# Kernel tuning notes

Measured on AMD Instinct MI355X. Metric: run time of the kernel, lower is better.

## Reference

```python
import jax, jax.numpy as jnp
import numpy as np

GAMMA = 0.99
LAMBDA = 0.95
NU = 0.001
LOG_2PI = float(np.log(2.0 * np.pi))

B, T, H, R, C, A = 256, 64, 512, 32, 32, 64
H1, H2 = 1024, 1024
D = H + R * C  # critic input dim = hidden_state + flattened latent


def setup_inputs() -> dict:
    key = jax.random.key(0)
    ks = jax.random.split(key, 13)
    sc = lambda n: 1.0 / np.sqrt(n)
    return {
        "h": jax.random.normal(ks[0], (B, T, H), jnp.float32),
        "z": jax.random.normal(ks[1], (B, T, R, C), jnp.float32),
        "reward": jax.random.normal(ks[2], (B, T, 1), jnp.float32) * 0.1,
        "cont": jax.random.uniform(ks[3], (B, T, 1), jnp.float32),
        "action": jax.random.normal(ks[4], (B, T, A), jnp.float32),
        "a_mu": jax.random.normal(ks[5], (B, T, A), jnp.float32),
        "a_sigma": jax.random.uniform(ks[6], (B, T, A), jnp.float32) + 0.5,
        "W1": jax.random.normal(ks[7], (D, H1), jnp.float32) * sc(D),
        "b1": jnp.zeros((H1,), jnp.float32),
        "W2": jax.random.normal(ks[8], (H1, H2), jnp.float32) * sc(H1),
        "b2": jnp.zeros((H2,), jnp.float32),
        "W3": jax.random.normal(ks[9], (H2, 1), jnp.float32) * sc(H2),
        "b3": jnp.zeros((1,), jnp.float32),
    }


def _critic(h, z, W1, b1, W2, b2, W3, b3):
    # flatten latent [B,T,R,C] -> [B,T,R*C], concat with hidden state
    zf = z.reshape(z.shape[0], z.shape[1], -1)
    st = jnp.concatenate([h, zf], axis=-1)  # [B,T,D]
    x = jax.nn.silu(st @ W1 + b1)
    x = jax.nn.silu(x @ W2 + b2)
    return x @ W3 + b3  # [B,T,1]


def _r_lambda(value, reward, cont):
    # value/reward/cont: [B,T,1]; backward TD(lambda) recursion over time
    vt = value[..., 0].T   # [T,B] time-major
    rt = reward[..., 0].T
    ct = cont[..., 0].T

    def step(R_next, xs):
        r, c, v_next = xs
        R_cur = r + GAMMA * c * ((1.0 - LAMBDA) * v_next + LAMBDA * R_next)
        return R_cur, R_cur

    _, Rs = jax.lax.scan(step, vt[-1], (rt[:-1], ct[:-1], vt[1:]), reverse=True)
    R_lam = jnp.concatenate([Rs, vt[-1:]], axis=0)  # [T,B]
    return R_lam.T[..., None]  # [B,T,1]


def reference(h, z, reward, cont, action, a_mu, a_sigma, W1, b1, W2, b2, W3, b3):
    value = _critic(h, z, W1, b1, W2, b2, W3, b3)  # [B,T,1]
    # R_lambda uses detached value estimates
    R_lam = _r_lambda(jax.lax.stop_gradient(value), reward, cont)  # [B,T,1]
    advantage = R_lam - value  # [B,T,1]

    # Normal(mu, sigma) log_prob and entropy
    log_sig = jnp.log(a_sigma)
    log_prob = -0.5 * jnp.square((action - a_mu) / a_sigma) - log_sig - 0.5 * LOG_2PI  # [B,T,A]
    entropy = 0.5 + 0.5 * LOG_2PI + log_sig  # [B,T,A]

    loss_actor = -jnp.mean(
        log_prob * jax.lax.stop_gradient(advantage)
        + NU * jax.lax.stop_gradient(entropy)
    )
    loss_critic = jnp.mean(0.5 * jnp.square(value - jax.lax.stop_gradient(R_lam)))
    return jnp.stack([loss_actor, loss_critic])
```

## Files before the change

kernel.cpp:

```cpp
#include <hip/hip_runtime.h>
#include <hip/hip_bf16.h>
#include <stdint.h>

typedef short s8v  __attribute__((ext_vector_type(8)));
typedef float f4v  __attribute__((ext_vector_type(4)));

__device__ __forceinline__ unsigned short f2bf(float f) {
  unsigned int u = __float_as_uint(f);
  u += 0x7fffu + ((u >> 16) & 1u);
  return (unsigned short)(u >> 16);
}
__device__ __forceinline__ float bf2f(unsigned short u) {
  return __uint_as_float(((unsigned int)u) << 16);
}

#define GLOAD16(g, l)                                                          \
  __builtin_amdgcn_global_load_lds(                                            \
      (const __attribute__((address_space(1))) unsigned int*)(g),              \
      (__attribute__((address_space(3))) unsigned int*)(l), 16, 0, 0)

__global__ __launch_bounds__(256) void prep_x(const float* __restrict__ h,
                                              const float* __restrict__ z,
                                              unsigned short* __restrict__ X) {
  int idx = blockIdx.x * 256 + threadIdx.x;
  int m = idx / 192;
  int c = (idx - m * 192) * 8;
  const float* s = (c < 512) ? (h + (size_t)m * 512 + c)
                             : (z + (size_t)m * 1024 + (c - 512));
  f4v f0 = *(const f4v*)s;
  f4v f1 = *(const f4v*)(s + 4);
  s8v o;
  o[0] = (short)f2bf(f0[0]); o[1] = (short)f2bf(f0[1]);
  o[2] = (short)f2bf(f0[2]); o[3] = (short)f2bf(f0[3]);
  o[4] = (short)f2bf(f1[0]); o[5] = (short)f2bf(f1[1]);
  o[6] = (short)f2bf(f1[2]); o[7] = (short)f2bf(f1[3]);
  *(s8v*)(X + (size_t)m * 1536 + c) = o;
}

__global__ __launch_bounds__(256) void transpose_w(const float* __restrict__ W,
                                                   unsigned short* __restrict__ WT,
                                                   int K, int N) {
  __shared__ float tile[32][33];
  int tx = threadIdx.x & 31;
  int ty = threadIdx.x >> 5;
  int k0 = blockIdx.x * 32;
  int n0 = blockIdx.y * 32;
#pragma unroll
  for (int i = 0; i < 4; ++i)
    tile[ty + i * 8][tx] = W[(size_t)(k0 + ty + i * 8) * N + n0 + tx];
  __syncthreads();
#pragma unroll
  for (int i = 0; i < 4; ++i)
    WT[(size_t)(n0 + ty + i * 8) * K + k0 + tx] = f2bf(tile[tx][ty + i * 8]);
}

template<int K, bool FUSE>
__global__ __launch_bounds__(512) void gemm256(
    const unsigned short* __restrict__ A, const unsigned short* __restrict__ Bt,
    const float* __restrict__ bias, unsigned short* __restrict__ Cout,
    const float* __restrict__ W3, float* __restrict__ value) {
  constexpr int NOUT = 1024;
  constexpr int NT = K / 64;
  __shared__ char lds[131072];
  char* const A0 = lds;
  char* const B0 = lds + 32768;
  char* const A1 = lds + 65536;
  char* const B1 = lds + 98304;

  const int tid = threadIdx.x;
  const int w = tid >> 6, l = tid & 63;
  const int wr = w >> 2, wc = w & 3;
  const int tm = blockIdx.x * 256;
  const int tn = blockIdx.y * 256;
  const int l15 = l & 15, lh = l >> 4;

  const int sgrow = tid >> 3;
  const int sgk = ((tid & 7) ^ (sgrow & 7)) * 8;
  const unsigned short* Ag = A  + (size_t)(tm + sgrow) * K + sgk;
  const unsigned short* Bg = Bt + (size_t)(tn + sgrow) * K + sgk;
  const int wb = w * 1024;

  f4v acc[8][4];
#pragma unroll
  for (int i = 0; i < 8; ++i)
#pragma unroll
    for (int j = 0; j < 4; ++j) acc[i][j] = (f4v){0.f, 0.f, 0.f, 0.f};

#pragma unroll
  for (int i = 0; i < 4; ++i) {
    GLOAD16(Ag + (size_t)i * 64 * K, A0 + i * 8192 + wb);
    GLOAD16(Bg + (size_t)i * 64 * K, B0 + i * 8192 + wb);
  }
  asm volatile("s_waitcnt vmcnt(0)" ::: "memory");
  __builtin_amdgcn_s_barrier();

  auto iter = [&](int t, char* Ac, char* Bc, char* An, char* Bn) {
    if (t + 1 < NT) {
      const size_t ko = (size_t)(t + 1) * 64;
#pragma unroll
      for (int i = 0; i < 4; ++i) {
        GLOAD16(Ag + (size_t)i * 64 * K + ko, An + i * 8192 + wb);
        GLOAD16(Bg + (size_t)i * 64 * K + ko, Bn + i * 8192 + wb);
      }
    }
    s8v bf[4];
#pragma unroll
    for (int ph = 0; ph < 4; ++ph) {
      const int kk = ph >> 1, mh = ph & 1;
      const int k16 = kk * 4 + lh;
      if (mh == 0) {
#pragma unroll
        for (int ni = 0; ni < 4; ++ni) {
          const int row = wc * 64 + ni * 16 + l15;
          bf[ni] = *(const s8v*)(Bc + row * 128 + ((k16 ^ (row & 7)) << 4));
        }
      }
      s8v af[4];
#pragma unroll
      for (int mi = 0; mi < 4; ++mi) {
        const int row = wr * 128 + (mh * 4 + mi) * 16 + l15;
        af[mi] = *(const s8v*)(Ac + row * 128 + ((k16 ^ (row & 7)) << 4));
      }
      __builtin_amdgcn_s_setprio(1);
#pragma unroll
      for (int mi = 0; mi < 4; ++mi)
#pragma unroll
        for (int ni = 0; ni < 4; ++ni)
          acc[mh * 4 + mi][ni] = __builtin_amdgcn_mfma_f32_16x16x32_bf16(
              af[mi], bf[ni], acc[mh * 4 + mi][ni], 0, 0, 0);
      __builtin_amdgcn_s_setprio(0);
      __builtin_amdgcn_s_barrier();
    }
    asm volatile("s_waitcnt vmcnt(0)" ::: "memory");
    __builtin_amdgcn_s_barrier();
  };

  for (int t = 0; t < NT; t += 2) {
    iter(t,     A0, B0, A1, B1);
    iter(t + 1, A1, B1, A0, B0);
  }

  if constexpr (!FUSE) {
#pragma unroll
    for (int ni = 0; ni < 4; ++ni) {
      const int col = tn + wc * 64 + ni * 16 + l15;
      const float bb = bias[col];
#pragma unroll
      for (int mi = 0; mi < 8; ++mi) {
#pragma unroll
        for (int r = 0; r < 4; ++r) {
          const int row = tm + wr * 128 + mi * 16 + lh * 4 + r;
          float v = acc[mi][ni][r] + bb;
          v = v / (1.f + __expf(-v));
          Cout[(size_t)row * NOUT + col] = f2bf(v);
        }
      }
    }
  } else {
    float bb[4], w3[4];
#pragma unroll
    for (int ni = 0; ni < 4; ++ni) {
      const int col = tn + wc * 64 + ni * 16 + l15;
      bb[ni] = bias[col];
      w3[ni] = W3[col];
    }
#pragma unroll
    for (int mi = 0; mi < 8; ++mi) {
#pragma unroll
      for (int r = 0; r < 4; ++r) {
        float s = 0.f;
#pragma unroll
        for (int ni = 0; ni < 4; ++ni) {
          float v = acc[mi][ni][r] + bb[ni];
          v = v / (1.f + __expf(-v));
          s += v * w3[ni];
        }
        s += __shfl_xor(s, 1);
        s += __shfl_xor(s, 2);
        s += __shfl_xor(s, 4);
        s += __shfl_xor(s, 8);
        if (l15 == 0)
          atomicAdd(&value[tm + wr * 128 + mi * 16 + lh * 4 + r], s);
      }
    }
  }
}

__global__ void td_kernel(const float* __restrict__ value,
                          const float* __restrict__ reward,
                          const float* __restrict__ cont,
                          const float* __restrict__ b3,
                          float* __restrict__ adv, float* __restrict__ accs) {
  const int b = threadIdx.x;
  const float g = 0.99f, lam = 0.95f;
  const float vb = b3[0];
  float Rn = value[b * 64 + 63] + vb;
  adv[b * 64 + 63] = 0.f;
  float s = 0.f;
  for (int t = 62; t >= 0; --t) {
    const int i = b * 64 + t;
    float vn = value[i + 1] + vb;
    float R = reward[i] + g * cont[i] * ((1.f - lam) * vn + lam * Rn);
    float a = R - (value[i] + vb);
    adv[i] = a;
    s += a * a;
    Rn = R;
  }
#pragma unroll
  for (int off = 32; off; off >>= 1) s += __shfl_down(s, off);
  __shared__ float red[4];
  if ((threadIdx.x & 63) == 0) red[threadIdx.x >> 6] = s;
  __syncthreads();
  if (threadIdx.x == 0) accs[0] = red[0] + red[1] + red[2] + red[3];
}

__global__ __launch_bounds__(256) void actor_kernel(
    const float* __restrict__ action, const float* __restrict__ a_mu,
    const float* __restrict__ a_sigma, const float* __restrict__ adv,
    float* __restrict__ accs) {
  const float C1 = 0.91893853320467274f;
  const float NU = 0.001f;
  const size_t t = (size_t)blockIdx.x * 256 + threadIdx.x;
  const size_t base = t * 4;
  const int m = (int)(base >> 6);
  const float av = adv[m];
  f4v a = *(const f4v*)(action + base);
  f4v mu = *(const f4v*)(a_mu + base);
  f4v sg = *(const f4v*)(a_sigma + base);
  float s = 0.f;
#pragma unroll
  for (int j = 0; j < 4; ++j) {
    float d = (a[j] - mu[j]) / sg[j];
    float ls = __logf(sg[j]);
    float lp = -0.5f * d * d - ls - C1;
    s += lp * av + NU * (0.5f + C1 + ls);
  }
#pragma unroll
  for (int off = 32; off; off >>= 1) s += __shfl_down(s, off);
  __shared__ float red[4];
  if ((threadIdx.x & 63) == 0) red[threadIdx.x >> 6] = s;
  __syncthreads();
  if (threadIdx.x == 0) atomicAdd(&accs[1], red[0] + red[1] + red[2] + red[3]);
}

__global__ void fin_kernel(const float* __restrict__ accs, float* __restrict__ out) {
  out[0] = -accs[1] / 1048576.0f;
  out[1] = 0.5f * accs[0] / 16384.0f;
}

extern "C" void kernel_launch(void* const* d_in, const int* in_sizes, int n_in,
                              void* d_out, int out_size, void* d_ws, size_t ws_size,
                              hipStream_t stream) {
  const float* h       = (const float*)d_in[0];
  const float* z       = (const float*)d_in[1];
  const float* reward  = (const float*)d_in[2];
  const float* cont    = (const float*)d_in[3];
  const float* action  = (const float*)d_in[4];
  const float* a_mu    = (const float*)d_in[5];
  const float* a_sigma = (const float*)d_in[6];
  const float* W1      = (const float*)d_in[7];
  const float* b1      = (const float*)d_in[8];
  const float* W2      = (const float*)d_in[9];
  const float* b2      = (const float*)d_in[10];
  const float* W3      = (const float*)d_in[11];
  const float* b3      = (const float*)d_in[12];

  char* ws = (char*)d_ws;
  unsigned short* X   = (unsigned short*)(ws);
  unsigned short* W1T = (unsigned short*)(ws + 50331648);
  unsigned short* W2T = (unsigned short*)(ws + 53477376);
  unsigned short* X1  = (unsigned short*)(ws + 55574528);
  float* value = (float*)(ws + 89128960);
  float* adv   = (float*)(ws + 89194496);
  float* accs  = (float*)(ws + 89260032);

  hipMemsetAsync(value, 0, 131088, stream);
  prep_x<<<12288, 256, 0, stream>>>(h, z, X);
  transpose_w<<<dim3(48, 32), 256, 0, stream>>>(W1, W1T, 1536, 1024);
  transpose_w<<<dim3(32, 32), 256, 0, stream>>>(W2, W2T, 1024, 1024);
  gemm256<1536, false><<<dim3(64, 4), 512, 0, stream>>>(X, W1T, b1, X1, nullptr, nullptr);
  gemm256<1024, true><<<dim3(64, 4), 512, 0, stream>>>(X1, W2T, b2, nullptr, W3, value);
  td_kernel<<<1, 256, 0, stream>>>(value, reward, cont, b3, adv, accs);
  actor_kernel<<<1024, 256, 0, stream>>>(action, a_mu, a_sigma, adv, accs);
  fin_kernel<<<1, 1, 0, stream>>>(accs, (float*)d_out);
}
```

Measured before the change: 290.0 us.

## Interleave next-tile loads across MFMA phases and fuse TD with actor loss

The GEMM main loop no longer issues all prefetch loads for the next K-tile at the top of each iteration. It now spreads them across the four MFMA phases, one quarter-tile per phase, and waits only at the last phase, so global-to-LDS traffic overlaps more evenly with compute. Separately, the serial single-block TD(lambda) kernel and the actor reduction kernel are merged into one kernel with one block per batch row. Each block computes its row's advantages in shared memory and then reduces the actor loss for that row, which removes one launch and the global advantage buffer. The risks are extra barriers per phase in the GEMM and a single-thread serial recursion inside each block.

```diff
diff --git a/kernel.cpp b/kernel.cpp
--- a/kernel.cpp
+++ b/kernel.cpp
@@ -9,9 +9,6 @@
   unsigned int u = __float_as_uint(f);
   u += 0x7fffu + ((u >> 16) & 1u);
   return (unsigned short)(u >> 16);
-}
-__device__ __forceinline__ float bf2f(unsigned short u) {
-  return __uint_as_float(((unsigned int)u) << 16);
 }
 
 #define GLOAD16(g, l)                                                          \
@@ -62,10 +59,6 @@
   constexpr int NOUT = 1024;
   constexpr int NT = K / 64;
   __shared__ char lds[131072];
-  char* const A0 = lds;
-  char* const B0 = lds + 32768;
-  char* const A1 = lds + 65536;
-  char* const B1 = lds + 98304;
 
   const int tid = threadIdx.x;
   const int w = tid >> 6, l = tid & 63;
@@ -74,12 +67,20 @@
   const int tn = blockIdx.y * 256;
   const int l15 = l & 15, lh = l >> 4;
 
-  const int sgrow = tid >> 3;
-  const int sgk = ((tid & 7) ^ (sgrow & 7)) * 8;
-  const unsigned short* Ag = A  + (size_t)(tm + sgrow) * K + sgk;
-  const unsigned short* Bg = Bt + (size_t)(tn + sgrow) * K + sgk;
+  const int srow = tid >> 3;
+  const int sk = ((tid & 7) ^ (srow & 7)) * 8;
+  const unsigned short* Ag = A  + (size_t)(tm + srow) * K + sk;
+  const unsigned short* Bg = Bt + (size_t)(tn + srow) * K + sk;
   const int wb = w * 1024;
 
+  auto stage_ht = [&](int p, char* bufbase, int kt) {
+    const unsigned short* g =
+        (p < 2 ? Ag : Bg) + (size_t)(p & 1) * 128 * K + kt;
+    char* d = bufbase + p * 16384 + wb;
+    GLOAD16(g, d);
+    GLOAD16(g + (size_t)64 * K, d + 8192);
+  };
+
   f4v acc[8][4];
 #pragma unroll
   for (int i = 0; i < 8; ++i)
@@ -87,23 +88,18 @@
     for (int j = 0; j < 4; ++j) acc[i][j] = (f4v){0.f, 0.f, 0.f, 0.f};
 
 #pragma unroll
-  for (int i = 0; i < 4; ++i) {
-    GLOAD16(Ag + (size_t)i * 64 * K, A0 + i * 8192 + wb);
-    GLOAD16(Bg + (size_t)i * 64 * K, B0 + i * 8192 + wb);
-  }
+  for (int p = 0; p < 4; ++p) stage_ht(p, lds, 0);
   asm volatile("s_waitcnt vmcnt(0)" ::: "memory");
   __builtin_amdgcn_s_barrier();
 
-  auto iter = [&](int t, char* Ac, char* Bc, char* An, char* Bn) {
-    if (t + 1 < NT) {
-      const size_t ko = (size_t)(t + 1) * 64;
-#pragma unroll
-      for (int i = 0; i < 4; ++i) {
-        GLOAD16(Ag + (size_t)i * 64 * K + ko, An + i * 8192 + wb);
-        GLOAD16(Bg + (size_t)i * 64 * K + ko, Bn + i * 8192 + wb);
-      }
-    }
-    s8v bf[4];
+  s8v bf[4];
+  for (int t = 0; t < NT; ++t) {
+    char* const cb = lds + ((t & 1) ? 65536 : 0);
+    char* const nb = lds + ((t & 1) ? 0 : 65536);
+    char* const Ab = cb;
+    char* const Bb = cb + 32768;
+    const bool st = (t + 1 < NT);
+    const int nkt = (t + 1) * 64;
 #pragma unroll
     for (int ph = 0; ph < 4; ++ph) {
       const int kk = ph >> 1, mh = ph & 1;
@@ -112,15 +108,17 @@
 #pragma unroll
         for (int ni = 0; ni < 4; ++ni) {
           const int row = wc * 64 + ni * 16 + l15;
-          bf[ni] = *(const s8v*)(Bc + row * 128 + ((k16 ^ (row & 7)) << 4));
+          bf[ni] = *(const s8v*)(Bb + row * 128 + ((k16 ^ (row & 7)) << 4));
         }
       }
       s8v af[4];
 #pragma unroll
       for (int mi = 0; mi < 4; ++mi) {
         const int row = wr * 128 + (mh * 4 + mi) * 16 + l15;
-        af[mi] = *(const s8v*)(Ac + row * 128 + ((k16 ^ (row & 7)) << 4));
-      }
+        af[mi] = *(const s8v*)(Ab + row * 128 + ((k16 ^ (row & 7)) << 4));
+      }
+      if (st) stage_ht(ph, nb, nkt);
+      __builtin_amdgcn_s_barrier();
       __builtin_amdgcn_s_setprio(1);
 #pragma unroll
       for (int mi = 0; mi < 4; ++mi)
@@ -129,15 +127,10 @@
           acc[mh * 4 + mi][ni] = __builtin_amdgcn_mfma_f32_16x16x32_bf16(
               af[mi], bf[ni], acc[mh * 4 + mi][ni], 0, 0, 0);
       __builtin_amdgcn_s_setprio(0);
+      if (ph == 3)
+        asm volatile("s_waitcnt vmcnt(0)" ::: "memory");
       __builtin_amdgcn_s_barrier();
     }
-    asm volatile("s_waitcnt vmcnt(0)" ::: "memory");
-    __builtin_amdgcn_s_barrier();
-  };
-
-  for (int t = 0; t < NT; t += 2) {
-    iter(t,     A0, B0, A1, B1);
-    iter(t + 1, A1, B1, A0, B0);
   }
 
   if constexpr (!FUSE) {
@@ -186,61 +179,58 @@
   }
 }
 
-__global__ void td_kernel(const float* __restrict__ value,
-                          const float* __restrict__ reward,
-                          const float* __restrict__ cont,
-                          const float* __restrict__ b3,
-                          float* __restrict__ adv, float* __restrict__ accs) {
-  const int b = threadIdx.x;
-  const float g = 0.99f, lam = 0.95f;
-  const float vb = b3[0];
-  float Rn = value[b * 64 + 63] + vb;
-  adv[b * 64 + 63] = 0.f;
+__global__ __launch_bounds__(256) void td_actor(
+    const float* __restrict__ value, const float* __restrict__ reward,
+    const float* __restrict__ cont, const float* __restrict__ b3,
+    const float* __restrict__ action, const float* __restrict__ a_mu,
+    const float* __restrict__ a_sigma, float* __restrict__ accs) {
+  __shared__ float vv[64], rr[64], cc[64], adv_s[64];
+  const int b = blockIdx.x, tid = threadIdx.x;
+  if (tid < 64) {
+    vv[tid] = value[b * 64 + tid] + b3[0];
+    rr[tid] = reward[b * 64 + tid];
+    cc[tid] = cont[b * 64 + tid];
+  }
+  __syncthreads();
+  if (tid == 0) {
+    const float g = 0.99f, lam = 0.95f;
+    float Rn = vv[63];
+    adv_s[63] = 0.f;
+    float s2 = 0.f;
+    for (int t = 62; t >= 0; --t) {
+      float R = rr[t] + g * cc[t] * ((1.f - lam) * vv[t + 1] + lam * Rn);
+      float a = R - vv[t];
+      adv_s[t] = a;
+      s2 += a * a;
+      Rn = R;
+    }
+    atomicAdd(&accs[0], s2);
+  }
+  __syncthreads();
+  const float C1 = 0.91893853320467274f;
+  const float NU = 0.001f;
+  const float av = adv_s[tid >> 2];
+  const size_t base = (size_t)b * 4096 + tid * 16;
   float s = 0.f;
-  for (int t = 62; t >= 0; --t) {
-    const int i = b * 64 + t;
-    float vn = value[i + 1] + vb;
-    float R = reward[i] + g * cont[i] * ((1.f - lam) * vn + lam * Rn);
-    float a = R - (value[i] + vb);
-    adv[i] = a;
-    s += a * a;
-    Rn = R;
+#pragma unroll
+  for (int j = 0; j < 4; ++j) {
+    f4v a  = *(const f4v*)(action  + base + j * 4);
+    f4v mu = *(const f4v*)(a_mu    + base + j * 4);
+    f4v sg = *(const f4v*)(a_sigma + base + j * 4);
+#pragma unroll
+    for (int i = 0; i < 4; ++i) {
+      float d = (a[i] - mu[i]) / sg[i];
+      float ls = __logf(sg[i]);
+      float lp = -0.5f * d * d - ls - C1;
+      s += lp * av + NU * (0.5f + C1 + ls);
+    }
   }
 #pragma unroll
   for (int off = 32; off; off >>= 1) s += __shfl_down(s, off);
   __shared__ float red[4];
-  if ((threadIdx.x & 63) == 0) red[threadIdx.x >> 6] = s;
-  __syncthreads();
-  if (threadIdx.x == 0) accs[0] = red[0] + red[1] + red[2] + red[3];
-}
-
-__global__ __launch_bounds__(256) void actor_kernel(
-    const float* __restrict__ action, const float* __restrict__ a_mu,
-    const float* __restrict__ a_sigma, const float* __restrict__ adv,
-    float* __restrict__ accs) {
-  const float C1 = 0.91893853320467274f;
-  const float NU = 0.001f;
-  const size_t t = (size_t)blockIdx.x * 256 + threadIdx.x;
-  const size_t base = t * 4;
-  const int m = (int)(base >> 6);
-  const float av = adv[m];
-  f4v a = *(const f4v*)(action + base);
-  f4v mu = *(const f4v*)(a_mu + base);
-  f4v sg = *(const f4v*)(a_sigma + base);
-  float s = 0.f;
-#pragma unroll
-  for (int j = 0; j < 4; ++j) {
-    float d = (a[j] - mu[j]) / sg[j];
-    float ls = __logf(sg[j]);
-    float lp = -0.5f * d * d - ls - C1;
-    s += lp * av + NU * (0.5f + C1 + ls);
-  }
-#pragma unroll
-  for (int off = 32; off; off >>= 1) s += __shfl_down(s, off);
-  __shared__ float red[4];
-  if ((threadIdx.x & 63) == 0) red[threadIdx.x >> 6] = s;
-  __syncthreads();
-  if (threadIdx.x == 0) atomicAdd(&accs[1], red[0] + red[1] + red[2] + red[3]);
+  if ((tid & 63) == 0) red[tid >> 6] = s;
+  __syncthreads();
+  if (tid == 0) atomicAdd(&accs[1], red[0] + red[1] + red[2] + red[3]);
 }
 
 __global__ void fin_kernel(const float* __restrict__ accs, float* __restrict__ out) {
@@ -271,16 +261,14 @@
   unsigned short* W2T = (unsigned short*)(ws + 53477376);
   unsigned short* X1  = (unsigned short*)(ws + 55574528);
   float* value = (float*)(ws + 89128960);
-  float* adv   = (float*)(ws + 89194496);
-  float* accs  = (float*)(ws + 89260032);
-
-  hipMemsetAsync(value, 0, 131088, stream);
+  float* accs  = (float*)(ws + 89194496);
+
+  hipMemsetAsync(value, 0, 65552, stream);
   prep_x<<<12288, 256, 0, stream>>>(h, z, X);
   transpose_w<<<dim3(48, 32), 256, 0, stream>>>(W1, W1T, 1536, 1024);
   transpose_w<<<dim3(32, 32), 256, 0, stream>>>(W2, W2T, 1024, 1024);
   gemm256<1536, false><<<dim3(64, 4), 512, 0, stream>>>(X, W1T, b1, X1, nullptr, nullptr);
   gemm256<1024, true><<<dim3(64, 4), 512, 0, stream>>>(X1, W2T, b2, nullptr, W3, value);
-  td_kernel<<<1, 256, 0, stream>>>(value, reward, cont, b3, adv, accs);
-  actor_kernel<<<1024, 256, 0, stream>>>(action, a_mu, a_sigma, adv, accs);
+  td_actor<<<256, 256, 0, stream>>>(value, reward, cont, b3, action, a_mu, a_sigma, accs);
   fin_kernel<<<1, 1, 0, stream>>>(accs, (float*)d_out);
 }
```

Result: faster. 273.4 us (-5.7%).
